# Performance work log

Hardware: AMD Instinct MI355X
Metric: run time of the kernel (lower is better)

Reference implementation:

```python
import jax, jax.numpy as jnp
import numpy as np

B, H, T, K, V = 2, 8, 2048, 128, 128


def setup_inputs() -> dict:
    key = jax.random.key(0)
    k1, k2, k3, k4, k5 = jax.random.split(key, 5)
    return {
        "q": jax.random.normal(k1, (B, H, T, K), dtype=jnp.float32),
        "k": jax.random.normal(k2, (B, H, T, K), dtype=jnp.float32),
        "v": jax.random.normal(k3, (B, H, T, V), dtype=jnp.float32),
        "i_gate": jax.random.normal(k4, (B, H, T), dtype=jnp.float32),
        "f_gate": jax.random.normal(k5, (B, H, T), dtype=jnp.float32),
    }


def reference(q, k, v, i_gate, f_gate):
    # Stabilized parallel mLSTM (same math as the chunked Triton kernel,
    # expressed in natural-log base instead of base-2).
    Bq, Hq, Tq, Kd = q.shape
    scale = Kd ** -0.5
    logf = jax.nn.log_sigmoid(f_gate)                      # [B,H,T]
    fc = jnp.cumsum(logf, axis=-1)                         # cumulative forget logits
    # log decay matrix: logD[t,s] = i[s] + (fc[t] - fc[s]) for s <= t
    logD = fc[..., :, None] - fc[..., None, :] + i_gate[..., None, :]  # [B,H,T,T]
    mask = jnp.tril(jnp.ones((Tq, Tq), dtype=bool))
    logD_masked = jnp.where(mask, logD, -jnp.inf)
    m = jnp.max(logD_masked, axis=-1)                      # row-wise stabilizer [B,H,T]
    D = jnp.where(mask, jnp.exp(logD - m[..., None]), 0.0) # stabilized decay matrix
    S = jnp.einsum("bhtk,bhsk->bhts", q, k) * scale * D    # gated scores
    norm = jnp.maximum(jnp.abs(jnp.sum(S, axis=-1)), jnp.exp(-m))  # [B,H,T]
    h = jnp.einsum("bhts,bhsv->bhtv", S, v) / norm[..., None]
    return h
```

## Files before the change

kernel.cpp:

```cpp
#include <hip/hip_runtime.h>

#define T_SEQ 2048
#define DHEAD 128
#define NBH 16
#define SCALE 0.08838834764831845f

typedef unsigned short u16;
typedef unsigned int u32;
typedef u16 u16x4 __attribute__((ext_vector_type(4)));
typedef u16 u16x8 __attribute__((ext_vector_type(8)));
typedef u32 u32x4 __attribute__((ext_vector_type(4)));
typedef __bf16 bf16x8 __attribute__((ext_vector_type(8)));
typedef float f32x16 __attribute__((ext_vector_type(16)));

__device__ __forceinline__ u16 f2bfu(float x) {
  union { float f; unsigned u; } c; c.f = x;
  unsigned u = c.u;
  u = u + 0x7FFFu + ((u >> 16) & 1u);
  return (u16)(u >> 16);
}

__device__ __forceinline__ u32 packbf2(float lo, float hi) {
  return (u32)f2bfu(lo) | ((u32)f2bfu(hi) << 16);
}

__device__ __forceinline__ bf16x8 ldsFrag(const u16* p) {
  u16x8 t = *(const u16x8*)p;
  return __builtin_bit_cast(bf16x8, t);
}

__device__ __forceinline__ void gld_lds16(const void* g, void* l) {
  __builtin_amdgcn_global_load_lds(
      (__attribute__((address_space(1))) const unsigned int*)g,
      (__attribute__((address_space(3))) unsigned int*)l, 16, 0, 0);
}

__global__ __launch_bounds__(256) void gate_scan_kernel(
    const float* __restrict__ ig, const float* __restrict__ fg,
    float* __restrict__ a_out, float* __restrict__ c_out,
    float* __restrict__ fc_out)
{
  const int bh  = blockIdx.x;
  const int tid = threadIdx.x;
  const int base = bh * T_SEQ + tid * 8;
  __shared__ float sbuf[256];

  float lf[8];
  float run = 0.f;
#pragma unroll
  for (int j = 0; j < 8; ++j) {
    float x  = fg[base + j];
    float ls = fminf(x, 0.f) - log1pf(expf(-fabsf(x)));
    run += ls; lf[j] = run;
  }
  sbuf[tid] = run; __syncthreads();
  for (int off = 1; off < 256; off <<= 1) {
    float t = (tid >= off) ? sbuf[tid - off] : 0.f;
    __syncthreads();
    sbuf[tid] += t;
    __syncthreads();
  }
  const float excl = (tid > 0) ? sbuf[tid - 1] : 0.f;
  __syncthreads();

  float fc[8], cm[8];
  float runm = -INFINITY;
#pragma unroll
  for (int j = 0; j < 8; ++j) {
    fc[j] = excl + lf[j];
    fc_out[base + j] = fc[j];
    float av = ig[base + j] - fc[j];
    a_out[base + j] = av;
    runm = fmaxf(runm, av);
    cm[j] = runm;
  }
  sbuf[tid] = runm; __syncthreads();
  for (int off = 1; off < 256; off <<= 1) {
    float t = (tid >= off) ? sbuf[tid - off] : -INFINITY;
    __syncthreads();
    sbuf[tid] = fmaxf(sbuf[tid], t);
    __syncthreads();
  }
  const float exclm = (tid > 0) ? sbuf[tid - 1] : -INFINITY;
#pragma unroll
  for (int j = 0; j < 8; ++j) {
    c_out[base + j] = fmaxf(exclm, cm[j]);
  }
}

__global__ __launch_bounds__(256) void cvt_k_kernel(
    const float* __restrict__ src, const float* __restrict__ ag,
    const float* __restrict__ cg, u16* __restrict__ dst)
{
  const int i = (blockIdx.x * 256 + threadIdx.x) * 4;
  const int bhs = i >> 7;
  const float sc = __expf(ag[bhs] - cg[bhs | 63]);
  const float4 x = *(const float4*)(src + i);
  u16x4 p;
  p[0] = f2bfu(x.x * sc); p[1] = f2bfu(x.y * sc);
  p[2] = f2bfu(x.z * sc); p[3] = f2bfu(x.w * sc);
  *(u16x4*)(dst + i) = p;
}

__global__ __launch_bounds__(256) void cvt_vt_kernel(
    const float* __restrict__ v, u16* __restrict__ vt)
{
  const int bh = blockIdx.y, kt = blockIdx.x, tid = threadIdx.x;
  __shared__ __align__(16) u16 L[128 * 72];
  const int n0 = (tid & 31) * 4, k0 = (tid >> 5) * 8;
  const float* vp = v + ((size_t)bh * T_SEQ + kt * 64 + k0) * DHEAD + n0;
  u16 tv[4][8];
#pragma unroll
  for (int rr = 0; rr < 8; ++rr) {
    const float4 x = *(const float4*)(vp + rr * DHEAD);
    tv[0][rr] = f2bfu(x.x); tv[1][rr] = f2bfu(x.y);
    tv[2][rr] = f2bfu(x.z); tv[3][rr] = f2bfu(x.w);
  }
#pragma unroll
  for (int j = 0; j < 4; ++j) {
    u16x8 p;
#pragma unroll
    for (int rr = 0; rr < 8; ++rr) p[rr] = tv[j][rr];
    *(u16x8*)(&L[(n0 + j) * 72 + k0]) = p;
  }
  __syncthreads();
  const int row = tid >> 1, s0 = (tid & 1) * 32;
  u16* op = vt + ((size_t)bh * DHEAD + row) * T_SEQ + kt * 64 + s0;
#pragma unroll
  for (int i = 0; i < 4; ++i)
    *(u16x8*)(op + i * 8) = *(const u16x8*)(&L[row * 72 + s0 + i * 8]);
}

template <bool FAST>
__global__ __launch_bounds__(512, 1) void mlstm_fwd_kernel(
    const float* __restrict__ qg, const float* __restrict__ kg,
    const float* __restrict__ vg,
    const u16* __restrict__ kbf, const u16* __restrict__ vtbf,
    const float* __restrict__ ag, const float* __restrict__ cg,
    const float* __restrict__ fcg, float* __restrict__ out)
{
  const int bx = (int)blockIdx.x;
  const int bh = bx & 15, p = bx >> 4;
  const int tid = (int)threadIdx.x;
  const int w8 = tid >> 6, lane = tid & 63;
  const int hh = lane >> 5, l32 = lane & 31;

  const int qsel  = w8 >> 2;
  const int half  = (w8 >> 1) & 1;
  const int strip = w8 & 1;
  const int qt    = qsel ? p : (31 - p);
  const int nST   = 32 - p;
  const int qrow0 = qt * 64 + strip * 32;
  const int qrowg = qrow0 + l32;

  __shared__ __align__(16) unsigned char SM[65536];
  __shared__ float rsh[128];

  const size_t hoff = (size_t)bh * T_SEQ * DHEAD;
  const int goff = bh * T_SEQ;

  bf16x8 qf[8];
  {
    const float* qp = qg + hoff + (size_t)qrowg * DHEAD + hh * 8;
#pragma unroll
    for (int ks = 0; ks < 8; ++ks) {
      const float4 x0 = *(const float4*)(qp + ks * 16);
      const float4 x1 = *(const float4*)(qp + ks * 16 + 4);
      u16x8 t;
      t[0] = f2bfu(x0.x); t[1] = f2bfu(x0.y); t[2] = f2bfu(x0.z); t[3] = f2bfu(x0.w);
      t[4] = f2bfu(x1.x); t[5] = f2bfu(x1.y); t[6] = f2bfu(x1.z); t[7] = f2bfu(x1.w);
      qf[ks] = __builtin_bit_cast(bf16x8, t);
    }
  }
  const float cmax = cg[goff + qt * 64 + 63];

  f32x16 oa[4];
#pragma unroll
  for (int nt = 0; nt < 4; ++nt)
#pragma unroll
    for (int r = 0; r < 16; ++r) oa[nt][r] = 0.f;
  float rsacc = 0.f;

  float kr[2][8], vr[2][8];

  auto stage_issue = [&](int st, int b) {
    if (FAST) {
      const u16* ks = kbf + ((size_t)goff + st * 64) * DHEAD;
      const u16* vs = vtbf + (size_t)bh * DHEAD * T_SEQ + st * 64;
#pragma unroll
      for (int j = 0; j < 2; ++j) {
        const int B = (w8 * 2 + j) * 64 + lane;
        {
          const int key = B >> 4;
          const int db = (B & 15) ^ (key & 7);
          gld_lds16(ks + (size_t)key * DHEAD + db * 8,
                    (u16*)(SM + b * 32768) + (w8 * 2 + j) * 512);
        }
        {
          const int n = B >> 3;
          const int kb = (B & 7) ^ (n & 7);
          gld_lds16(vs + (size_t)n * T_SEQ + kb * 8,
                    (u16*)(SM + b * 32768 + 16384) + (w8 * 2 + j) * 512);
        }
      }
    } else {
      const float ct = cg[goff + st * 64 + 63];
      const float* kp = kg + hoff + (size_t)(st * 64) * DHEAD;
      const float* vp = vg + hoff + (size_t)(st * 64) * DHEAD;
#pragma unroll
      for (int j = 0; j < 2; ++j) {
        const int B = (w8 * 2 + j) * 64 + lane;
        const int key = B >> 4;
        const int db = (B & 15) ^ (key & 7);
        const float sc = __expf(ag[goff + st * 64 + key] - ct);
        const float4 x0 = *(const float4*)(kp + (size_t)key * DHEAD + db * 8);
        const float4 x1 = *(const float4*)(kp + (size_t)key * DHEAD + db * 8 + 4);
        kr[j][0] = x0.x * sc; kr[j][1] = x0.y * sc; kr[j][2] = x0.z * sc; kr[j][3] = x0.w * sc;
        kr[j][4] = x1.x * sc; kr[j][5] = x1.y * sc; kr[j][6] = x1.z * sc; kr[j][7] = x1.w * sc;
        const int n = B >> 3;
        const int kb = (B & 7) ^ (n & 7);
#pragma unroll
        for (int rr = 0; rr < 8; ++rr)
          vr[j][rr] = vp[(size_t)(kb * 8 + rr) * DHEAD + n];
      }
    }
  };
  auto stage_commit = [&](int b) {
    if (!FAST) {
#pragma unroll
      for (int j = 0; j < 2; ++j) {
        const int B = (w8 * 2 + j) * 64 + lane;
        u16x8 pk, pw;
#pragma unroll
        for (int rr = 0; rr < 8; ++rr) { pk[rr] = f2bfu(kr[j][rr]); pw[rr] = f2bfu(vr[j][rr]); }
        *(u16x8*)((u16*)(SM + b * 32768) + B * 8) = pk;
        *(u16x8*)((u16*)(SM + b * 32768 + 16384) + B * 8) = pw;
      }
    }
  };

  stage_issue(0, 0);
  stage_commit(0);
  __syncthreads();

  for (int st = 0; st < nST; ++st) {
    const int b = st & 1;
    if (st + 1 < nST) stage_issue(st + 1, b ^ 1);

    const bool act = (qsel == 0) || (st <= qt);
    if (act) {
      const u16* Kb_ = (const u16*)(SM + b * 32768);
      const u16* Vb_ = (const u16*)(SM + b * 32768 + 16384);
      const int keyl = half * 32 + l32;

      f32x16 s0, s1;
#pragma unroll
      for (int r = 0; r < 16; ++r) { s0[r] = 0.f; s1[r] = 0.f; }
#pragma unroll
      for (int k2 = 0; k2 < 4; ++k2) {
        {
          const int db = 2 * (2 * k2) + hh;
          const bf16x8 kf = ldsFrag(Kb_ + keyl * 128 + ((db ^ (keyl & 7)) * 8));
          s0 = __builtin_amdgcn_mfma_f32_32x32x16_bf16(kf, qf[2 * k2], s0, 0, 0, 0);
        }
        {
          const int db = 2 * (2 * k2 + 1) + hh;
          const bf16x8 kf = ldsFrag(Kb_ + keyl * 128 + ((db ^ (keyl & 7)) * 8));
          s1 = __builtin_amdgcn_mfma_f32_32x32x16_bf16(kf, qf[2 * k2 + 1], s1, 0, 0, 0);
        }
      }
      const float etile = SCALE * __expf(cg[goff + st * 64 + 63] - cmax);
      const bool diag = (st == qt);

      float pv[16];
      float r0 = 0.f, r1 = 0.f, r2 = 0.f, r3 = 0.f;
#pragma unroll
      for (int reg = 0; reg < 16; ++reg) {
        float x = (s0[reg] + s1[reg]) * etile;
        if (diag) {
          const int rowl = (reg & 3) + 8 * (reg >> 2) + 4 * hh;
          if (st * 64 + half * 32 + rowl > qrowg) x = 0.f;
        }
        pv[reg] = x;
        if ((reg & 3) == 0) r0 += x; else if ((reg & 3) == 1) r1 += x;
        else if ((reg & 3) == 2) r2 += x; else r3 += x;
      }
      rsacc += (r0 + r1) + (r2 + r3);

      u32 d8[8];
#pragma unroll
      for (int q = 0; q < 4; ++q) {
        d8[2 * q]     = packbf2(pv[4 * q],     pv[4 * q + 1]);
        d8[2 * q + 1] = packbf2(pv[4 * q + 2], pv[4 * q + 3]);
      }
#pragma unroll
      for (int k2 = 0; k2 < 2; ++k2) {
        const int qo = 2 * k2 + (hh ^ 1), qn = 2 * k2 + hh;
        const u32 e0 = __shfl_xor(d8[2 * qo], 32, 64);
        const u32 e1 = __shfl_xor(d8[2 * qo + 1], 32, 64);
        const u32x4 fw = hh ? (u32x4){e0, e1, d8[2 * qn], d8[2 * qn + 1]}
                            : (u32x4){d8[2 * qn], d8[2 * qn + 1], e0, e1};
        const bf16x8 pfrag = __builtin_bit_cast(bf16x8, fw);
        const int kb = half * 4 + k2 * 2 + hh;
#pragma unroll
        for (int nt = 0; nt < 4; ++nt) {
          const int n = nt * 32 + l32;
          const bf16x8 vf = ldsFrag(Vb_ + n * 64 + ((kb ^ (n & 7)) * 8));
          oa[nt] = __builtin_amdgcn_mfma_f32_32x32x16_bf16(vf, pfrag, oa[nt], 0, 0, 0);
        }
      }
    }
    if (st + 1 < nST) stage_commit(b ^ 1);
    __syncthreads();
  }

  rsacc += __shfl_xor(rsacc, 32, 64);
  const int combo = qsel * 2 + strip;
  float* osh = (float*)SM;

  if (half == 1) {
#pragma unroll
    for (int nt = 0; nt < 4; ++nt)
#pragma unroll
      for (int reg = 0; reg < 16; ++reg) {
        const int rown = (reg & 3) + 8 * (reg >> 2) + 4 * hh;
        osh[combo * 4096 + (nt * 32 + rown) * 32 + l32] = oa[nt][reg];
      }
    if (hh == 0) rsh[combo * 32 + l32] = rsacc;
  }
  __syncthreads();
  if (half == 0) {
    const float rstot = rsacc + rsh[combo * 32 + l32];
    const float nf = __expf(-(cmax + fcg[goff + qrowg]));
    const float inv = 1.f / fmaxf(fabsf(rstot), nf);
    float* op = out + hoff + (size_t)qrowg * DHEAD;
#pragma unroll
    for (int nt = 0; nt < 4; ++nt)
#pragma unroll
      for (int q = 0; q < 4; ++q) {
        float4 ov;
        const int base = combo * 4096 + (nt * 32 + 8 * q + 4 * hh) * 32 + l32;
        ov.x = (oa[nt][4 * q]     + osh[base])      * inv;
        ov.y = (oa[nt][4 * q + 1] + osh[base + 32]) * inv;
        ov.z = (oa[nt][4 * q + 2] + osh[base + 64]) * inv;
        ov.w = (oa[nt][4 * q + 3] + osh[base + 96]) * inv;
        *(float4*)(op + nt * 32 + 8 * q + 4 * hh) = ov;
      }
  }
}

extern "C" void kernel_launch(void* const* d_in, const int* in_sizes, int n_in,
                              void* d_out, int out_size, void* d_ws, size_t ws_size,
                              hipStream_t stream) {
  const float* q  = (const float*)d_in[0];
  const float* k  = (const float*)d_in[1];
  const float* v  = (const float*)d_in[2];
  const float* ig = (const float*)d_in[3];
  const float* fg = (const float*)d_in[4];

  const size_t gate_bytes = (size_t)3 * NBH * T_SEQ * sizeof(float);
  const size_t kv_elems   = (size_t)NBH * T_SEQ * DHEAD;
  const bool fast = ws_size >= gate_bytes + 2 * kv_elems * sizeof(u16);

  float* a_ws  = (float*)d_ws;
  float* c_ws  = a_ws + NBH * T_SEQ;
  float* fc_ws = c_ws + NBH * T_SEQ;
  u16* kbf  = (u16*)((char*)d_ws + gate_bytes);
  u16* vtbf = kbf + kv_elems;

  gate_scan_kernel<<<dim3(NBH), dim3(256), 0, stream>>>(ig, fg, a_ws, c_ws, fc_ws);
  if (fast) {
    cvt_k_kernel<<<dim3((unsigned)(kv_elems / 1024)), dim3(256), 0, stream>>>(
        k, a_ws, c_ws, kbf);
    cvt_vt_kernel<<<dim3(T_SEQ / 64, NBH), dim3(256), 0, stream>>>(v, vtbf);
    mlstm_fwd_kernel<true><<<dim3(256), dim3(512), 0, stream>>>(
        q, k, v, kbf, vtbf, a_ws, c_ws, fc_ws, (float*)d_out);
  } else {
    mlstm_fwd_kernel<false><<<dim3(256), dim3(512), 0, stream>>>(
        q, k, v, kbf, vtbf, a_ws, c_ws, fc_ws, (float*)d_out);
  }
}
```

Measured before the change: 165.9 us.

## Split key tile across waves with 16x16 MFMAs and LDS output reduction

Each wave now owns a 16-key slice of the 64-key tile and computes scores for all 64 query rows with 16x16x32 MFMAs, then feeds bf16 probabilities straight into 16x16x16 MFMAs for the PV product. This drops the cross-half shuffles and the register staging in the non-fast path. Waves that share a query tile then reduce their partial outputs and row sums serially through padded LDS before a coalesced store. The cost is a larger per-wave accumulator (32 f32x4 tiles), four serialized reduction rounds with barriers, and more LDS traffic at the end.

```diff
diff --git a/kernel.cpp b/kernel.cpp
--- a/kernel.cpp
+++ b/kernel.cpp
@@ -9,9 +9,10 @@
 typedef unsigned int u32;
 typedef u16 u16x4 __attribute__((ext_vector_type(4)));
 typedef u16 u16x8 __attribute__((ext_vector_type(8)));
-typedef u32 u32x4 __attribute__((ext_vector_type(4)));
+typedef u32 u32x2 __attribute__((ext_vector_type(2)));
+typedef short s16x4 __attribute__((ext_vector_type(4)));
 typedef __bf16 bf16x8 __attribute__((ext_vector_type(8)));
-typedef float f32x16 __attribute__((ext_vector_type(16)));
+typedef float f32x4 __attribute__((ext_vector_type(4)));
 
 __device__ __forceinline__ u16 f2bfu(float x) {
   union { float f; unsigned u; } c; c.f = x;
@@ -27,6 +28,15 @@
 __device__ __forceinline__ bf16x8 ldsFrag(const u16* p) {
   u16x8 t = *(const u16x8*)p;
   return __builtin_bit_cast(bf16x8, t);
+}
+
+__device__ __forceinline__ f32x4 mfma16x16x16bf16(s16x4 a, s16x4 b, f32x4 c) {
+#if __has_builtin(__builtin_amdgcn_mfma_f32_16x16x16bf16_1k)
+  return __builtin_amdgcn_mfma_f32_16x16x16bf16_1k(a, b, c, 0, 0, 0);
+#else
+  asm("v_mfma_f32_16x16x16_bf16 %0, %1, %2, %0" : "+v"(c) : "v"(a), "v"(b));
+  return c;
+#endif
 }
 
 __device__ __forceinline__ void gld_lds16(const void* g, void* l) {
@@ -133,7 +143,7 @@
 
 template <bool FAST>
 __global__ __launch_bounds__(512, 1) void mlstm_fwd_kernel(
-    const float* __restrict__ qg, const float* __restrict__ kg,
+    const float* __restrict__ qg, const float* __restrict__ kxg,
     const float* __restrict__ vg,
     const u16* __restrict__ kbf, const u16* __restrict__ vtbf,
     const float* __restrict__ ag, const float* __restrict__ cg,
@@ -143,209 +153,206 @@
   const int bh = bx & 15, p = bx >> 4;
   const int tid = (int)threadIdx.x;
   const int w8 = tid >> 6, lane = tid & 63;
-  const int hh = lane >> 5, l32 = lane & 31;
-
-  const int qsel  = w8 >> 2;
-  const int half  = (w8 >> 1) & 1;
-  const int strip = w8 & 1;
-  const int qt    = qsel ? p : (31 - p);
-  const int nST   = 32 - p;
-  const int qrow0 = qt * 64 + strip * 32;
-  const int qrowg = qrow0 + l32;
-
-  __shared__ __align__(16) unsigned char SM[65536];
-  __shared__ float rsh[128];
+  const int quad = lane >> 4, l16 = lane & 15;
+
+  const int qsel = w8 >> 2;
+  const int kg4  = w8 & 3;
+  const int qt   = qsel ? p : (31 - p);
+  const int nST  = 32 - p;
+  const int qrow0 = qt * 64;
+
+  __shared__ __align__(16) unsigned char SM[68096];
 
   const size_t hoff = (size_t)bh * T_SEQ * DHEAD;
   const int goff = bh * T_SEQ;
 
-  bf16x8 qf[8];
-  {
-    const float* qp = qg + hoff + (size_t)qrowg * DHEAD + hh * 8;
-#pragma unroll
-    for (int ks = 0; ks < 8; ++ks) {
-      const float4 x0 = *(const float4*)(qp + ks * 16);
-      const float4 x1 = *(const float4*)(qp + ks * 16 + 4);
+  bf16x8 qf[16];
+#pragma unroll
+  for (int nt = 0; nt < 4; ++nt) {
+    const float* qp = qg + hoff + (size_t)(qrow0 + nt * 16 + l16) * DHEAD + quad * 8;
+#pragma unroll
+    for (int kc = 0; kc < 4; ++kc) {
+      const float4 x0 = *(const float4*)(qp + kc * 32);
+      const float4 x1 = *(const float4*)(qp + kc * 32 + 4);
       u16x8 t;
       t[0] = f2bfu(x0.x); t[1] = f2bfu(x0.y); t[2] = f2bfu(x0.z); t[3] = f2bfu(x0.w);
       t[4] = f2bfu(x1.x); t[5] = f2bfu(x1.y); t[6] = f2bfu(x1.z); t[7] = f2bfu(x1.w);
-      qf[ks] = __builtin_bit_cast(bf16x8, t);
+      qf[nt * 4 + kc] = __builtin_bit_cast(bf16x8, t);
     }
   }
   const float cmax = cg[goff + qt * 64 + 63];
 
-  f32x16 oa[4];
-#pragma unroll
-  for (int nt = 0; nt < 4; ++nt)
-#pragma unroll
-    for (int r = 0; r < 16; ++r) oa[nt][r] = 0.f;
-  float rsacc = 0.f;
-
-  float kr[2][8], vr[2][8];
-
-  auto stage_issue = [&](int st, int b) {
+  f32x4 oa[8][4];
+#pragma unroll
+  for (int mt = 0; mt < 8; ++mt)
+#pragma unroll
+    for (int nt = 0; nt < 4; ++nt) oa[mt][nt] = (f32x4){0.f, 0.f, 0.f, 0.f};
+  float rsacc[4] = {0.f, 0.f, 0.f, 0.f};
+
+  auto stage = [&](int st) {
+    const int b = st & 1;
+    u16* KbL = (u16*)(SM + b * 16384);
+    u16* VbL = (u16*)(SM + 32768 + b * 16384);
     if (FAST) {
       const u16* ks = kbf + ((size_t)goff + st * 64) * DHEAD;
       const u16* vs = vtbf + (size_t)bh * DHEAD * T_SEQ + st * 64;
 #pragma unroll
       for (int j = 0; j < 2; ++j) {
         const int B = (w8 * 2 + j) * 64 + lane;
-        {
-          const int key = B >> 4;
-          const int db = (B & 15) ^ (key & 7);
-          gld_lds16(ks + (size_t)key * DHEAD + db * 8,
-                    (u16*)(SM + b * 32768) + (w8 * 2 + j) * 512);
-        }
-        {
-          const int n = B >> 3;
-          const int kb = (B & 7) ^ (n & 7);
-          gld_lds16(vs + (size_t)n * T_SEQ + kb * 8,
-                    (u16*)(SM + b * 32768 + 16384) + (w8 * 2 + j) * 512);
-        }
+        { const int key = B >> 4; const int db = (B & 15) ^ (key & 7);
+          gld_lds16(ks + (size_t)key * DHEAD + db * 8, KbL + (w8 * 2 + j) * 512); }
+        { const int n = B >> 3; const int kb = (B & 7) ^ (n & 7);
+          gld_lds16(vs + (size_t)n * T_SEQ + kb * 8, VbL + (w8 * 2 + j) * 512); }
       }
     } else {
       const float ct = cg[goff + st * 64 + 63];
-      const float* kp = kg + hoff + (size_t)(st * 64) * DHEAD;
+      const float* kp = kxg + hoff + (size_t)(st * 64) * DHEAD;
       const float* vp = vg + hoff + (size_t)(st * 64) * DHEAD;
 #pragma unroll
       for (int j = 0; j < 2; ++j) {
         const int B = (w8 * 2 + j) * 64 + lane;
-        const int key = B >> 4;
-        const int db = (B & 15) ^ (key & 7);
-        const float sc = __expf(ag[goff + st * 64 + key] - ct);
-        const float4 x0 = *(const float4*)(kp + (size_t)key * DHEAD + db * 8);
-        const float4 x1 = *(const float4*)(kp + (size_t)key * DHEAD + db * 8 + 4);
-        kr[j][0] = x0.x * sc; kr[j][1] = x0.y * sc; kr[j][2] = x0.z * sc; kr[j][3] = x0.w * sc;
-        kr[j][4] = x1.x * sc; kr[j][5] = x1.y * sc; kr[j][6] = x1.z * sc; kr[j][7] = x1.w * sc;
-        const int n = B >> 3;
-        const int kb = (B & 7) ^ (n & 7);
-#pragma unroll
-        for (int rr = 0; rr < 8; ++rr)
-          vr[j][rr] = vp[(size_t)(kb * 8 + rr) * DHEAD + n];
+        { const int key = B >> 4; const int db = (B & 15) ^ (key & 7);
+          const float sc = __expf(ag[goff + st * 64 + key] - ct);
+          const float4 x0 = *(const float4*)(kp + (size_t)key * DHEAD + db * 8);
+          const float4 x1 = *(const float4*)(kp + (size_t)key * DHEAD + db * 8 + 4);
+          u16x8 pk;
+          pk[0] = f2bfu(x0.x * sc); pk[1] = f2bfu(x0.y * sc);
+          pk[2] = f2bfu(x0.z * sc); pk[3] = f2bfu(x0.w * sc);
+          pk[4] = f2bfu(x1.x * sc); pk[5] = f2bfu(x1.y * sc);
+          pk[6] = f2bfu(x1.z * sc); pk[7] = f2bfu(x1.w * sc);
+          *(u16x8*)(KbL + B * 8) = pk; }
+        { const int n = B >> 3; const int kb = (B & 7) ^ (n & 7);
+          u16x8 pw;
+#pragma unroll
+          for (int rr = 0; rr < 8; ++rr)
+            pw[rr] = f2bfu(vp[(size_t)(kb * 8 + rr) * DHEAD + n]);
+          *(u16x8*)(VbL + B * 8) = pw; }
       }
     }
   };
-  auto stage_commit = [&](int b) {
-    if (!FAST) {
-#pragma unroll
-      for (int j = 0; j < 2; ++j) {
-        const int B = (w8 * 2 + j) * 64 + lane;
-        u16x8 pk, pw;
-#pragma unroll
-        for (int rr = 0; rr < 8; ++rr) { pk[rr] = f2bfu(kr[j][rr]); pw[rr] = f2bfu(vr[j][rr]); }
-        *(u16x8*)((u16*)(SM + b * 32768) + B * 8) = pk;
-        *(u16x8*)((u16*)(SM + b * 32768 + 16384) + B * 8) = pw;
-      }
-    }
-  };
-
-  stage_issue(0, 0);
-  stage_commit(0);
+
+  stage(0);
   __syncthreads();
+
+  const int keyA = kg4 * 16 + l16;
+  const int ksw  = l16 & 7;
+  const int kbu  = kg4 * 2 + (quad >> 1);
+  const int kofs = (quad & 1) * 4;
 
   for (int st = 0; st < nST; ++st) {
     const int b = st & 1;
-    if (st + 1 < nST) stage_issue(st + 1, b ^ 1);
-
-    const bool act = (qsel == 0) || (st <= qt);
-    if (act) {
-      const u16* Kb_ = (const u16*)(SM + b * 32768);
-      const u16* Vb_ = (const u16*)(SM + b * 32768 + 16384);
-      const int keyl = half * 32 + l32;
-
-      f32x16 s0, s1;
-#pragma unroll
-      for (int r = 0; r < 16; ++r) { s0[r] = 0.f; s1[r] = 0.f; }
-#pragma unroll
-      for (int k2 = 0; k2 < 4; ++k2) {
-        {
-          const int db = 2 * (2 * k2) + hh;
-          const bf16x8 kf = ldsFrag(Kb_ + keyl * 128 + ((db ^ (keyl & 7)) * 8));
-          s0 = __builtin_amdgcn_mfma_f32_32x32x16_bf16(kf, qf[2 * k2], s0, 0, 0, 0);
-        }
-        {
-          const int db = 2 * (2 * k2 + 1) + hh;
-          const bf16x8 kf = ldsFrag(Kb_ + keyl * 128 + ((db ^ (keyl & 7)) * 8));
-          s1 = __builtin_amdgcn_mfma_f32_32x32x16_bf16(kf, qf[2 * k2 + 1], s1, 0, 0, 0);
-        }
-      }
+    if (st + 1 < nST) stage(st + 1);
+
+    if (st <= qt) {
+      const u16* KbL = (const u16*)(SM + b * 16384);
+      const u16* VbL = (const u16*)(SM + 32768 + b * 16384);
+
+      f32x4 sa[4];
+#pragma unroll
+      for (int nt = 0; nt < 4; ++nt) sa[nt] = (f32x4){0.f, 0.f, 0.f, 0.f};
+#pragma unroll
+      for (int kc = 0; kc < 4; ++kc) {
+        const bf16x8 kf = ldsFrag(KbL + keyA * 128 + (((kc * 4 + quad) ^ ksw) * 8));
+        sa[0] = __builtin_amdgcn_mfma_f32_16x16x32_bf16(kf, qf[0 * 4 + kc], sa[0], 0, 0, 0);
+        sa[1] = __builtin_amdgcn_mfma_f32_16x16x32_bf16(kf, qf[1 * 4 + kc], sa[1], 0, 0, 0);
+        sa[2] = __builtin_amdgcn_mfma_f32_16x16x32_bf16(kf, qf[2 * 4 + kc], sa[2], 0, 0, 0);
+        sa[3] = __builtin_amdgcn_mfma_f32_16x16x32_bf16(kf, qf[3 * 4 + kc], sa[3], 0, 0, 0);
+      }
+
       const float etile = SCALE * __expf(cg[goff + st * 64 + 63] - cmax);
       const bool diag = (st == qt);
 
-      float pv[16];
-      float r0 = 0.f, r1 = 0.f, r2 = 0.f, r3 = 0.f;
-#pragma unroll
-      for (int reg = 0; reg < 16; ++reg) {
-        float x = (s0[reg] + s1[reg]) * etile;
+      s16x4 pfr[4];
+#pragma unroll
+      for (int nt = 0; nt < 4; ++nt) {
+        float x0 = sa[nt][0] * etile, x1 = sa[nt][1] * etile;
+        float x2 = sa[nt][2] * etile, x3 = sa[nt][3] * etile;
         if (diag) {
-          const int rowl = (reg & 3) + 8 * (reg >> 2) + 4 * hh;
-          if (st * 64 + half * 32 + rowl > qrowg) x = 0.f;
+          const int qr = nt * 16 + l16, kb0 = kg4 * 16 + quad * 4;
+          if (kb0 + 0 > qr) x0 = 0.f;
+          if (kb0 + 1 > qr) x1 = 0.f;
+          if (kb0 + 2 > qr) x2 = 0.f;
+          if (kb0 + 3 > qr) x3 = 0.f;
         }
-        pv[reg] = x;
-        if ((reg & 3) == 0) r0 += x; else if ((reg & 3) == 1) r1 += x;
-        else if ((reg & 3) == 2) r2 += x; else r3 += x;
-      }
-      rsacc += (r0 + r1) + (r2 + r3);
-
-      u32 d8[8];
-#pragma unroll
-      for (int q = 0; q < 4; ++q) {
-        d8[2 * q]     = packbf2(pv[4 * q],     pv[4 * q + 1]);
-        d8[2 * q + 1] = packbf2(pv[4 * q + 2], pv[4 * q + 3]);
-      }
-#pragma unroll
-      for (int k2 = 0; k2 < 2; ++k2) {
-        const int qo = 2 * k2 + (hh ^ 1), qn = 2 * k2 + hh;
-        const u32 e0 = __shfl_xor(d8[2 * qo], 32, 64);
-        const u32 e1 = __shfl_xor(d8[2 * qo + 1], 32, 64);
-        const u32x4 fw = hh ? (u32x4){e0, e1, d8[2 * qn], d8[2 * qn + 1]}
-                            : (u32x4){d8[2 * qn], d8[2 * qn + 1], e0, e1};
-        const bf16x8 pfrag = __builtin_bit_cast(bf16x8, fw);
-        const int kb = half * 4 + k2 * 2 + hh;
-#pragma unroll
-        for (int nt = 0; nt < 4; ++nt) {
-          const int n = nt * 32 + l32;
-          const bf16x8 vf = ldsFrag(Vb_ + n * 64 + ((kb ^ (n & 7)) * 8));
-          oa[nt] = __builtin_amdgcn_mfma_f32_32x32x16_bf16(vf, pfrag, oa[nt], 0, 0, 0);
-        }
-      }
-    }
-    if (st + 1 < nST) stage_commit(b ^ 1);
-    __syncthreads();
-  }
-
-  rsacc += __shfl_xor(rsacc, 32, 64);
-  const int combo = qsel * 2 + strip;
+        rsacc[nt] += (x0 + x1) + (x2 + x3);
+        pfr[nt] = __builtin_bit_cast(s16x4, (u32x2){packbf2(x0, x1), packbf2(x2, x3)});
+      }
+
+#pragma unroll
+      for (int mt = 0; mt < 8; ++mt) {
+        const int vd = mt * 16 + l16;
+        const s16x4 va = *(const s16x4*)(VbL + vd * 64 + ((kbu ^ (vd & 7)) * 8) + kofs);
+        oa[mt][0] = mfma16x16x16bf16(va, pfr[0], oa[mt][0]);
+        oa[mt][1] = mfma16x16x16bf16(va, pfr[1], oa[mt][1]);
+        oa[mt][2] = mfma16x16x16bf16(va, pfr[2], oa[mt][2]);
+        oa[mt][3] = mfma16x16x16bf16(va, pfr[3], oa[mt][3]);
+      }
+    }
+    __syncthreads();
+  }
+
+  float rst[4];
+#pragma unroll
+  for (int nt = 0; nt < 4; ++nt) {
+    float x = rsacc[nt];
+    x += __shfl_xor(x, 16, 64);
+    x += __shfl_xor(x, 32, 64);
+    rst[nt] = x;
+  }
+  float* rshp = (float*)(SM + 66048);
+  if (lane < 16) {
+#pragma unroll
+    for (int nt = 0; nt < 4; ++nt)
+      rshp[qsel * 256 + kg4 * 64 + nt * 16 + lane] = rst[nt];
+  }
+  __syncthreads();
+
+  float inv[4] = {0.f, 0.f, 0.f, 0.f};
+  if (kg4 == 3) {
+#pragma unroll
+    for (int nt = 0; nt < 4; ++nt) {
+      const int row = nt * 16 + l16;
+      const float tot = rshp[qsel * 256 + row] + rshp[qsel * 256 + 64 + row]
+                      + rshp[qsel * 256 + 128 + row] + rshp[qsel * 256 + 192 + row];
+      const float nf = __expf(-(cmax + fcg[goff + qrow0 + row]));
+      inv[nt] = 1.f / fmaxf(fabsf(tot), nf);
+    }
+  }
+
   float* osh = (float*)SM;
-
-  if (half == 1) {
-#pragma unroll
-    for (int nt = 0; nt < 4; ++nt)
-#pragma unroll
-      for (int reg = 0; reg < 16; ++reg) {
-        const int rown = (reg & 3) + 8 * (reg >> 2) + 4 * hh;
-        osh[combo * 4096 + (nt * 32 + rown) * 32 + l32] = oa[nt][reg];
-      }
-    if (hh == 0) rsh[combo * 32 + l32] = rsacc;
-  }
-  __syncthreads();
-  if (half == 0) {
-    const float rstot = rsacc + rsh[combo * 32 + l32];
-    const float nf = __expf(-(cmax + fcg[goff + qrowg]));
-    const float inv = 1.f / fmaxf(fabsf(rstot), nf);
-    float* op = out + hoff + (size_t)qrowg * DHEAD;
-#pragma unroll
-    for (int nt = 0; nt < 4; ++nt)
-#pragma unroll
-      for (int q = 0; q < 4; ++q) {
-        float4 ov;
-        const int base = combo * 4096 + (nt * 32 + 8 * q + 4 * hh) * 32 + l32;
-        ov.x = (oa[nt][4 * q]     + osh[base])      * inv;
-        ov.y = (oa[nt][4 * q + 1] + osh[base + 32]) * inv;
-        ov.z = (oa[nt][4 * q + 2] + osh[base + 64]) * inv;
-        ov.w = (oa[nt][4 * q + 3] + osh[base + 96]) * inv;
-        *(float4*)(op + nt * 32 + 8 * q + 4 * hh) = ov;
-      }
+  const int obase = qsel * 64 * 129;
+  for (int r = 0; r < 4; ++r) {
+    if (kg4 == r) {
+#pragma unroll
+      for (int mt = 0; mt < 8; ++mt)
+#pragma unroll
+        for (int nt = 0; nt < 4; ++nt)
+#pragma unroll
+          for (int rg = 0; rg < 4; ++rg) {
+            const int row = nt * 16 + l16;
+            const int vd = mt * 16 + quad * 4 + rg;
+            const int ad = obase + row * 129 + vd;
+            float v = oa[mt][nt][rg];
+            if (r > 0) v += osh[ad];
+            if (r == 3) v *= inv[nt];
+            osh[ad] = v;
+          }
+    }
+    __syncthreads();
+  }
+
+  {
+    const int col = tid & 31;
+    const int rg0 = tid >> 5;
+#pragma unroll
+    for (int i = 0; i < 8; ++i) {
+      const int ra = rg0 + 16 * i;
+      const int tile = ra >> 6, row = ra & 63;
+      const int qtt = tile ? p : (31 - p);
+      const float* lp = osh + (tile * 64 + row) * 129 + col * 4;
+      float4 v; v.x = lp[0]; v.y = lp[1]; v.z = lp[2]; v.w = lp[3];
+      *(float4*)(out + hoff + (size_t)(qtt * 64 + row) * DHEAD + col * 4) = v;
+    }
   }
 }
 
```

New measurement: 150.3 us. 1.1x faster.
